# Performance work log

Hardware: AMD Instinct MI355X
Metric: run time of the kernel (lower is better)

## Reference

```python
import jax, jax.numpy as jnp
import numpy as np

N, E, G = 50000, 1600000, 512
IN, H = 16, 128


def setup_inputs() -> dict:
    key = jax.random.key(0)
    ks = jax.random.split(key, 10)
    x = jax.random.normal(ks[0], (N, IN), dtype=jnp.float32)
    edge_index = jax.random.randint(ks[1], (2, E), 0, N, dtype=jnp.int64)
    batch = jnp.sort(jax.random.randint(ks[2], (N,), 0, G, dtype=jnp.int64))
    s = lambda k, sh, fan: jax.random.normal(k, sh, dtype=jnp.float32) / np.sqrt(fan)
    return {
        "x": x, "edge_index": edge_index, "batch": batch,
        "W1": s(ks[3], (IN, H), IN), "b1": jnp.zeros((H,), jnp.float32),
        "W2": s(ks[4], (H, H), H), "b2": jnp.zeros((H,), jnp.float32),
        "Wlab": s(ks[5], (H, 1), H), "blab": jnp.zeros((1,), jnp.float32),
        "Wd1": s(ks[6], (H, 64), H), "bd1": jnp.zeros((64,), jnp.float32),
        "Wd2": s(ks[7], (64, 2), 64), "bd2": jnp.zeros((2,), jnp.float32),
    }


def _gcn_conv(x, src, dst, norm, W, b, num_nodes):
    # x' = sum_{(s,d) in E+selfloops} norm_e * (x W)[s] scattered to d, + b
    h = x @ W                                  # [N, H]
    msgs = h[src] * norm[:, None]              # [E+N, H]
    out = jax.ops.segment_sum(msgs, dst, num_segments=num_nodes)
    return out + b


def _forward(x, edge_index, batch, W1, b1, W2, b2, Wlab, blab, Wd1, bd1, Wd2, bd2):
    num_nodes = x.shape[0]
    loop = jnp.arange(num_nodes, dtype=edge_index.dtype)
    src = jnp.concatenate([edge_index[0], loop])
    dst = jnp.concatenate([edge_index[1], loop])
    # symmetric GCN normalization: deg computed at dst after self-loops
    deg = jax.ops.segment_sum(jnp.ones_like(dst, dtype=x.dtype), dst,
                              num_segments=num_nodes)
    dinv = jnp.where(deg > 0, jax.lax.rsqrt(deg), 0.0)
    norm = dinv[src] * dinv[dst]               # [E+N]

    h = jax.nn.relu(_gcn_conv(x, src, dst, norm, W1, b1, num_nodes))
    h = jax.nn.relu(_gcn_conv(h, src, dst, norm, W2, b2, num_nodes))

    # global mean pool over graphs
    sums = jax.ops.segment_sum(h, batch, num_segments=G)        # [G, H]
    cnts = jax.ops.segment_sum(jnp.ones((num_nodes,), h.dtype), batch,
                               num_segments=G)
    pooled = sums / jnp.maximum(cnts, 1.0)[:, None]

    label_out = jax.nn.sigmoid(pooled @ Wlab + blab)            # [G, 1]
    # grad_reverse is identity in the forward pass
    dom_out = jax.nn.relu(pooled @ Wd1 + bd1) @ Wd2 + bd2       # [G, 2]
    return label_out, dom_out


def reference(x, edge_index, batch, W1, b1, W2, b2, Wlab, blab, Wd1, bd1, Wd2, bd2):
    return _forward(x, edge_index, batch, W1, b1, W2, b2, Wlab, blab,
                    Wd1, bd1, Wd2, bd2)
```

## Files before the change

kernel.cpp:

```cpp
#include <hip/hip_runtime.h>
#include <math.h>


#define BCAP 12288

typedef __attribute__((ext_vector_type(8))) short short8;
typedef __attribute__((ext_vector_type(4))) float f32x4;

__device__ __forceinline__ void bf4acc(uint2 u, float* a) {
    a[0] += __uint_as_float(u.x << 16);
    a[1] += __uint_as_float(u.x & 0xffff0000u);
    a[2] += __uint_as_float(u.y << 16);
    a[3] += __uint_as_float(u.y & 0xffff0000u);
}

__device__ __forceinline__ unsigned short bf1(float a) {
    unsigned ua = __float_as_uint(a);
    return (unsigned short)((ua + 0x7fffu + ((ua >> 16) & 1u)) >> 16);
}

__global__ __launch_bounds__(256) void k_bfill(
        const int* __restrict__ ei, int* __restrict__ bcnt,
        unsigned* __restrict__ col1,
        const int* __restrict__ batch, int* __restrict__ gptr,
        float* __restrict__ gsum, const float* __restrict__ W2,
        unsigned short* __restrict__ W2bf,
        int E, int chunk, int NB, int N, int G) {
    __shared__ int bins[256];
    __shared__ int base[256];
    for (int t = threadIdx.x; t < NB; t += 256) bins[t] = 0;
    __syncthreads();
    const int e0 = blockIdx.x * chunk;
    int e1 = e0 + chunk; if (e1 > E) e1 = E;
    for (int j = e0 + (int)threadIdx.x; j < e1; j += 256)
        atomicAdd(&bins[ei[E + j] >> 8], 1);
    __syncthreads();
    for (int t = threadIdx.x; t < NB; t += 256) {
        base[t] = bins[t] ? atomicAdd(&bcnt[t], bins[t]) : 0;
        bins[t] = 0;
    }
    __syncthreads();
    for (int j = e0 + (int)threadIdx.x; j < e1; j += 256) {
        int d = ei[E + j];
        int s = ei[j];
        int b = d >> 8;
        int pos = base[b] + atomicAdd(&bins[b], 1);
        if (pos < BCAP)
            col1[(size_t)b * BCAP + pos] = ((unsigned)(d & 255) << 16) | (unsigned)s;
    }

    const int gid = blockIdx.x * 256 + threadIdx.x;
    const int gsz = gridDim.x * 256;
    for (int i = gid; i < G * 32; i += gsz)
        ((float4*)gsum)[i] = make_float4(0.f, 0.f, 0.f, 0.f);
    for (int i = gid; i < 16384; i += gsz) {
        const int f2 = i >> 7, f1 = i & 127;
        W2bf[i] = bf1(W2[f1 * 128 + f2]);
    }
    for (int g = gid; g <= G; g += gsz) {
        int lo = 0, hi = N;
        while (lo < hi) {
            int mid = (lo + hi) >> 1;
            if (batch[mid] < g) lo = mid + 1; else hi = mid;
        }
        gptr[g] = lo;
    }
}

__global__ __launch_bounds__(256) void k_bsort(const unsigned* __restrict__ col1,
                                               const int* __restrict__ bcnt,
                                               int* __restrict__ col,
                                               int* __restrict__ rowptr,
                                               float* __restrict__ dinv,
                                               const float* __restrict__ x,
                                               unsigned short* __restrict__ xsb,
                                               int N, int E, int NB) {
    __shared__ unsigned ec[BCAP];
    __shared__ int bins[256], sc[256];
    __shared__ float dvb[256];
    const int b = blockIdx.x, t = threadIdx.x;

    {
        int v = (t < NB) ? bcnt[t] : 0;
        bins[t] = v;
        __syncthreads();
        for (int off = 1; off < 256; off <<= 1) {
            int add = (t >= off) ? bins[t - off] : 0;
            __syncthreads();
            bins[t] += add;
            __syncthreads();
        }
    }
    const int s0 = (b == 0) ? 0 : bins[b - 1];
    int cnt = bcnt[b];
    if (cnt > BCAP) cnt = BCAP;
    __syncthreads();

    for (int i = t; i < cnt; i += 256) ec[i] = col1[(size_t)b * BCAP + i];
    bins[t] = 0;
    __syncthreads();
    for (int i = t; i < cnt; i += 256) atomicAdd(&bins[ec[i] >> 16], 1);
    __syncthreads();
    const int v = bins[t];
    sc[t] = v;
    __syncthreads();
    for (int off = 1; off < 256; off <<= 1) {
        int add = (t >= off) ? sc[t - off] : 0;
        __syncthreads();
        sc[t] += add;
        __syncthreads();
    }
    const int ex = sc[t] - v;
    __syncthreads();
    sc[t] = ex;
    bins[t] = 0;
    const float dv = rsqrtf((float)(v + 1));
    dvb[t] = dv;
    const int n0 = b * 256;
    if (n0 + t < N) {
        rowptr[n0 + t] = s0 + ex;
        dinv[n0 + t] = dv;
    }
    if (b == 0 && t == 0) rowptr[N] = E;
    __syncthreads();
    for (int i = t; i < cnt; i += 256) {
        unsigned e = ec[i];
        int dl = e >> 16;
        int p = sc[dl] + atomicAdd(&bins[dl], 1);
        col[s0 + p] = (int)(e & 0xffffu);
    }
    int nn = N - n0; if (nn > 256) nn = 256;
    const int lim = nn * 16;
    for (int i = t; i < lim; i += 256) {
        float vx = x[(size_t)n0 * 16 + i] * dvb[i >> 4];
        xsb[(size_t)n0 * 16 + i] = bf1(vx);
    }
}

__global__ __launch_bounds__(512, 4) void k_l12g(
        const int* __restrict__ rowptr, const int* __restrict__ col,
        const unsigned short* __restrict__ xsb,
        const float* __restrict__ dinv,
        const float* __restrict__ W1, const float* __restrict__ b1,
        const unsigned short* __restrict__ W2bf,
        unsigned short* __restrict__ ht1b, int N) {
    __shared__ __align__(16) unsigned short W2s[128 * 136];
    __shared__ __align__(16) unsigned short h1b[64 * 136];
    __shared__ __align__(16) float arow[64 * 16];
    __shared__ float dv[64];
    const int tid = threadIdx.x;
    const int n0 = blockIdx.x * 64;
    const int w = tid >> 6, lane = tid & 63;

    for (int i = tid; i < 2048; i += 512) {
        const int f2 = i >> 4, seg = i & 15;
        *(uint4*)&W2s[f2 * 136 + seg * 8] = ((const uint4*)W2bf)[i];
    }
    if (tid < 64) dv[tid] = (n0 + tid < N) ? dinv[n0 + tid] : 0.f;

    {
        const int nd = lane >> 3, sub = lane & 7;
        const int slot = sub >> 2, qq = sub & 3;
        const int j = w * 8 + nd;
        const int n = n0 + j;
        float a[4] = {0.f, 0.f, 0.f, 0.f};
        if (n < N) {
            const int r1 = rowptr[n + 1];
            for (int e = rowptr[n] + slot; e < r1; e += 2)
                bf4acc(*(const uint2*)(xsb + (size_t)col[e] * 16 + qq * 4), a);
        }
#pragma unroll
        for (int i = 0; i < 4; ++i) a[i] += __shfl_xor(a[i], 4);
        if (slot == 0) {
            if (n < N) {
                bf4acc(*(const uint2*)(xsb + (size_t)n * 16 + qq * 4), a);
                *(float4*)&arow[j * 16 + qq * 4] = make_float4(a[0], a[1], a[2], a[3]);
            } else {
                *(float4*)&arow[j * 16 + qq * 4] = make_float4(0.f, 0.f, 0.f, 0.f);
            }
        }
    }
    const int f = tid & 127, jg = tid >> 7;
    float w1r[16];
#pragma unroll
    for (int k = 0; k < 16; ++k) w1r[k] = W1[k * 128 + f];
    const float bias = b1[f];
    __syncthreads();

#pragma unroll 4
    for (int j = jg * 16; j < jg * 16 + 16; ++j) {
        float s = 0.f;
#pragma unroll
        for (int k = 0; k < 16; ++k) s += arow[j * 16 + k] * w1r[k];
        h1b[j * 136 + f] = bf1(fmaxf(dv[j] * s + bias, 0.f));
    }
    __syncthreads();

    const int mt = w & 3, nh = w >> 2;
    const int lm = lane & 15, quad = lane >> 4;
    f32x4 acc[4];
#pragma unroll
    for (int t = 0; t < 4; ++t) acc[t] = (f32x4){0.f, 0.f, 0.f, 0.f};
#pragma unroll
    for (int kb = 0; kb < 4; ++kb) {
        const short8 af = *(const short8*)&h1b[(mt * 16 + lm) * 136 + kb * 32 + quad * 8];
#pragma unroll
        for (int t = 0; t < 4; ++t) {
            const short8 bfv = *(const short8*)&W2s[(nh * 64 + t * 16 + lm) * 136 + kb * 32 + quad * 8];
            acc[t] = __builtin_amdgcn_mfma_f32_16x16x32_bf16(af, bfv, acc[t], 0, 0, 0);
        }
    }
#pragma unroll
    for (int t = 0; t < 4; ++t) {
        const int f2 = nh * 64 + t * 16 + lm;
#pragma unroll
        for (int r = 0; r < 4; ++r) {
            const int j = mt * 16 + quad * 4 + r;
            const int n = n0 + j;
            if (n < N)
                ht1b[(size_t)n * 128 + f2] = bf1(acc[t][r] * dv[j]);
        }
    }
}

__global__ __launch_bounds__(512) void k_gat128pool(
        const int* __restrict__ rowptr, const int* __restrict__ col,
        const unsigned short* __restrict__ ht1b,
        const float* __restrict__ dinv, const float* __restrict__ b2,
        const int* __restrict__ batch, float* __restrict__ gsum, int N) {
    __shared__ __align__(16) float h2s[8][128];
    __shared__ int bats[8];
    const int wave = threadIdx.x >> 6, lane = threadIdx.x & 63;
    const int half = lane >> 5, q = lane & 31;
    const int n = blockIdx.x * 8 + wave;
    float a[4] = {0.f, 0.f, 0.f, 0.f};
    if (n < N) {
        const int r0 = rowptr[n], r1 = rowptr[n + 1];
        int j = r0 + half;
        while (j + 6 < r1) {
            int s0 = col[j], s1 = col[j + 2], s2 = col[j + 4], s3 = col[j + 6];
            uint2 u0 = *(const uint2*)(ht1b + (size_t)s0 * 128 + q * 4);
            uint2 u1 = *(const uint2*)(ht1b + (size_t)s1 * 128 + q * 4);
            uint2 u2 = *(const uint2*)(ht1b + (size_t)s2 * 128 + q * 4);
            uint2 u3 = *(const uint2*)(ht1b + (size_t)s3 * 128 + q * 4);
            bf4acc(u0, a); bf4acc(u1, a); bf4acc(u2, a); bf4acc(u3, a);
            j += 8;
        }
        while (j < r1) {
            bf4acc(*(const uint2*)(ht1b + (size_t)col[j] * 128 + q * 4), a);
            j += 2;
        }
        if (half == 0)
            bf4acc(*(const uint2*)(ht1b + (size_t)n * 128 + q * 4), a);
    }
#pragma unroll
    for (int i = 0; i < 4; ++i) a[i] += __shfl_xor(a[i], 32);
    if (half == 0) {
        if (n < N) {
            const float d = dinv[n];
            const float4 bb = *(const float4*)(b2 + q * 4);
            h2s[wave][q * 4 + 0] = fmaxf(a[0] * d + bb.x, 0.f);
            h2s[wave][q * 4 + 1] = fmaxf(a[1] * d + bb.y, 0.f);
            h2s[wave][q * 4 + 2] = fmaxf(a[2] * d + bb.z, 0.f);
            h2s[wave][q * 4 + 3] = fmaxf(a[3] * d + bb.w, 0.f);
            if (q == 0) bats[wave] = batch[n];
        } else {
            h2s[wave][q * 4 + 0] = 0.f; h2s[wave][q * 4 + 1] = 0.f;
            h2s[wave][q * 4 + 2] = 0.f; h2s[wave][q * 4 + 3] = 0.f;
            if (q == 0) bats[wave] = -1;
        }
    }
    __syncthreads();
    if (threadIdx.x < 32) {
        const int qq = threadIdx.x;
        int bprev = bats[0];
        float4 acc4 = *(const float4*)&h2s[0][qq * 4];
#pragma unroll
        for (int wv = 1; wv < 8; ++wv) {
            const int bw = bats[wv];
            const float4 rv = *(const float4*)&h2s[wv][qq * 4];
            if (bw == bprev) {
                acc4.x += rv.x; acc4.y += rv.y; acc4.z += rv.z; acc4.w += rv.w;
            } else {
                if (bprev >= 0) {
                    float* gs = gsum + (size_t)bprev * 128 + qq * 4;
                    unsafeAtomicAdd(gs + 0, acc4.x); unsafeAtomicAdd(gs + 1, acc4.y);
                    unsafeAtomicAdd(gs + 2, acc4.z); unsafeAtomicAdd(gs + 3, acc4.w);
                }
                bprev = bw; acc4 = rv;
            }
        }
        if (bprev >= 0) {
            float* gs = gsum + (size_t)bprev * 128 + qq * 4;
            unsafeAtomicAdd(gs + 0, acc4.x); unsafeAtomicAdd(gs + 1, acc4.y);
            unsafeAtomicAdd(gs + 2, acc4.z); unsafeAtomicAdd(gs + 3, acc4.w);
        }
    }
}

__global__ __launch_bounds__(128) void k_head(
        const float* __restrict__ gsum, const int* __restrict__ gptr,
        const float* __restrict__ Wlab, const float* __restrict__ blab,
        const float* __restrict__ Wd1, const float* __restrict__ bd1,
        const float* __restrict__ Wd2, const float* __restrict__ bd2,
        float* __restrict__ out, int G) {
    __shared__ float sp[128];
    __shared__ float red[128];
    __shared__ float hd[64];
    const int g = blockIdx.x, t = threadIdx.x;
    const float cnt = (float)(gptr[g + 1] - gptr[g]);
    const float invc = 1.f / fmaxf(cnt, 1.f);
    const float pooled = gsum[g * 128 + t] * invc;
    sp[t] = pooled;
    red[t] = pooled * Wlab[t];
    __syncthreads();
    for (int off = 64; off > 0; off >>= 1) {
        if (t < off) red[t] += red[t + off];
        __syncthreads();
    }
    if (t == 0) {
        float z = red[0] + blab[0];
        out[g] = 1.f / (1.f + expf(-z));
    }
    if (t < 64) {
        float s = bd1[t];
        for (int f = 0; f < 128; ++f) s += sp[f] * Wd1[f * 64 + t];
        hd[t] = fmaxf(s, 0.f);
    }
    __syncthreads();
    if (t < 2) {
        float s = bd2[t];
        for (int j = 0; j < 64; ++j) s += hd[j] * Wd2[j * 2 + t];
        out[G + g * 2 + t] = s;
    }
}

extern "C" void kernel_launch(void* const* d_in, const int* in_sizes, int n_in,
                              void* d_out, int out_size, void* d_ws, size_t ws_size,
                              hipStream_t stream) {
    const float* x     = (const float*)d_in[0];
    const int*   ei    = (const int*)d_in[1];
    const int*   batch = (const int*)d_in[2];
    const float* W1    = (const float*)d_in[3];
    const float* b1    = (const float*)d_in[4];
    const float* W2    = (const float*)d_in[5];
    const float* b2    = (const float*)d_in[6];
    const float* Wlab  = (const float*)d_in[7];
    const float* blab  = (const float*)d_in[8];
    const float* Wd1   = (const float*)d_in[9];
    const float* bd1   = (const float*)d_in[10];
    const float* Wd2   = (const float*)d_in[11];
    const float* bd2   = (const float*)d_in[12];
    float* out = (float*)d_out;

    const int N = in_sizes[0] / 16;
    const int E = in_sizes[1] / 2;
    const int G = out_size / 3;
    const int NB = (N + 255) >> 8;

    char* p = (char*)d_ws;
    auto carve = [&](size_t bytes) {
        void* r = (void*)p;
        p += (bytes + 255) & ~(size_t)255;
        return r;
    };
    int*      bcnt   = (int*)     carve(256 * 4);
    unsigned* col1   = (unsigned*)carve((size_t)NB * BCAP * 4);
    int*      col    = (int*)     carve((size_t)E * 4);
    int*      rowptr = (int*)     carve((size_t)(N + 1) * 4);
    int*      gptr   = (int*)     carve((size_t)(G + 1) * 4);
    float*    dinv   = (float*)   carve((size_t)N * 4);
    unsigned short* xsb  = (unsigned short*)carve((size_t)N * 16 * 2);
    unsigned short* W2bf = (unsigned short*)carve(128 * 128 * 2);
    unsigned short* ht1b = (unsigned short*)carve((size_t)N * 128 * 2);
    float*    gsum   = (float*)   carve((size_t)G * 128 * 4);

    const int FB = 256;
    const int chunk = (E + FB - 1) / FB;

    hipMemsetAsync(bcnt, 0, 256 * 4, stream);
    k_bfill  <<<FB, 256, 0, stream>>>(ei, bcnt, col1, batch, gptr, gsum, W2,
                                      W2bf, E, chunk, NB, N, G);
    k_bsort  <<<NB, 256, 0, stream>>>(col1, bcnt, col, rowptr, dinv, x, xsb,
                                      N, E, NB);
    k_l12g   <<<(N + 63) / 64, 512, 0, stream>>>(rowptr, col, xsb, dinv,
                                                 W1, b1, W2bf, ht1b, N);
    k_gat128pool<<<(N + 7) / 8, 512, 0, stream>>>(rowptr, col, ht1b, dinv, b2,
                                                  batch, gsum, N);
    k_head   <<<G, 128, 0, stream>>>(gsum, gptr, Wlab, blab, Wd1, bd1, Wd2,
                                     bd2, out, G);
}
```

Measured before the change: 230.1 us.

## Split layer-2 gather-pool into two 64-column passes with 16-byte loads

The 128-feature neighbor gather-and-pool kernel is replaced by a kernel that handles one 64-column half of the features and is launched twice. Each wave now splits a node's edges over 8 lane groups and issues 16-byte loads per lane, so more edges are in flight and each pass touches a smaller slice of the bf16 feature table, which may fit the cache better. The cost is reading the CSR indices twice, two kernel launches, and more shuffle reductions.

```diff
diff --git a/kernel.cpp b/kernel.cpp
--- a/kernel.cpp
+++ b/kernel.cpp
@@ -12,6 +12,17 @@
     a[1] += __uint_as_float(u.x & 0xffff0000u);
     a[2] += __uint_as_float(u.y << 16);
     a[3] += __uint_as_float(u.y & 0xffff0000u);
+}
+
+__device__ __forceinline__ void bf8acc(uint4 u, float* a) {
+    a[0] += __uint_as_float(u.x << 16);
+    a[1] += __uint_as_float(u.x & 0xffff0000u);
+    a[2] += __uint_as_float(u.y << 16);
+    a[3] += __uint_as_float(u.y & 0xffff0000u);
+    a[4] += __uint_as_float(u.z << 16);
+    a[5] += __uint_as_float(u.z & 0xffff0000u);
+    a[6] += __uint_as_float(u.w << 16);
+    a[7] += __uint_as_float(u.w & 0xffff0000u);
 }
 
 __device__ __forceinline__ unsigned short bf1(float a) {
@@ -223,55 +234,69 @@
     }
 }
 
-__global__ __launch_bounds__(512) void k_gat128pool(
+__global__ __launch_bounds__(512) void k_gat64pool(
         const int* __restrict__ rowptr, const int* __restrict__ col,
         const unsigned short* __restrict__ ht1b,
         const float* __restrict__ dinv, const float* __restrict__ b2,
-        const int* __restrict__ batch, float* __restrict__ gsum, int N) {
-    __shared__ __align__(16) float h2s[8][128];
+        const int* __restrict__ batch, float* __restrict__ gsum,
+        int N, int c0) {
+    __shared__ __align__(16) float h2s[8][64];
     __shared__ int bats[8];
     const int wave = threadIdx.x >> 6, lane = threadIdx.x & 63;
-    const int half = lane >> 5, q = lane & 31;
+    const int oct = lane >> 3, t8 = lane & 7;
     const int n = blockIdx.x * 8 + wave;
-    float a[4] = {0.f, 0.f, 0.f, 0.f};
+    const unsigned short* hb = ht1b + c0 + t8 * 8;
+    float a[8] = {0.f, 0.f, 0.f, 0.f, 0.f, 0.f, 0.f, 0.f};
     if (n < N) {
-        const int r0 = rowptr[n], r1 = rowptr[n + 1];
-        int j = r0 + half;
-        while (j + 6 < r1) {
-            int s0 = col[j], s1 = col[j + 2], s2 = col[j + 4], s3 = col[j + 6];
-            uint2 u0 = *(const uint2*)(ht1b + (size_t)s0 * 128 + q * 4);
-            uint2 u1 = *(const uint2*)(ht1b + (size_t)s1 * 128 + q * 4);
-            uint2 u2 = *(const uint2*)(ht1b + (size_t)s2 * 128 + q * 4);
-            uint2 u3 = *(const uint2*)(ht1b + (size_t)s3 * 128 + q * 4);
-            bf4acc(u0, a); bf4acc(u1, a); bf4acc(u2, a); bf4acc(u3, a);
+        const int r1 = rowptr[n + 1];
+        int j = rowptr[n] + oct;
+        while (j + 24 < r1) {
+            const int s0 = col[j], s1 = col[j + 8];
+            const int s2 = col[j + 16], s3 = col[j + 24];
+            const uint4 u0 = *(const uint4*)(hb + (size_t)s0 * 128);
+            const uint4 u1 = *(const uint4*)(hb + (size_t)s1 * 128);
+            const uint4 u2 = *(const uint4*)(hb + (size_t)s2 * 128);
+            const uint4 u3 = *(const uint4*)(hb + (size_t)s3 * 128);
+            bf8acc(u0, a); bf8acc(u1, a); bf8acc(u2, a); bf8acc(u3, a);
+            j += 32;
+        }
+        while (j < r1) {
+            bf8acc(*(const uint4*)(hb + (size_t)col[j] * 128), a);
             j += 8;
         }
-        while (j < r1) {
-            bf4acc(*(const uint2*)(ht1b + (size_t)col[j] * 128 + q * 4), a);
-            j += 2;
-        }
-        if (half == 0)
-            bf4acc(*(const uint2*)(ht1b + (size_t)n * 128 + q * 4), a);
-    }
-#pragma unroll
-    for (int i = 0; i < 4; ++i) a[i] += __shfl_xor(a[i], 32);
-    if (half == 0) {
+        if (oct == 0)
+            bf8acc(*(const uint4*)(hb + (size_t)n * 128), a);
+    }
+#pragma unroll
+    for (int i = 0; i < 8; ++i) {
+        a[i] += __shfl_xor(a[i], 8);
+        a[i] += __shfl_xor(a[i], 16);
+        a[i] += __shfl_xor(a[i], 32);
+    }
+    if (oct == 0) {
         if (n < N) {
             const float d = dinv[n];
-            const float4 bb = *(const float4*)(b2 + q * 4);
-            h2s[wave][q * 4 + 0] = fmaxf(a[0] * d + bb.x, 0.f);
-            h2s[wave][q * 4 + 1] = fmaxf(a[1] * d + bb.y, 0.f);
-            h2s[wave][q * 4 + 2] = fmaxf(a[2] * d + bb.z, 0.f);
-            h2s[wave][q * 4 + 3] = fmaxf(a[3] * d + bb.w, 0.f);
-            if (q == 0) bats[wave] = batch[n];
+            const float4 bb0 = *(const float4*)(b2 + c0 + t8 * 8);
+            const float4 bb1 = *(const float4*)(b2 + c0 + t8 * 8 + 4);
+            const float4 v0 = make_float4(fmaxf(a[0] * d + bb0.x, 0.f),
+                                          fmaxf(a[1] * d + bb0.y, 0.f),
+                                          fmaxf(a[2] * d + bb0.z, 0.f),
+                                          fmaxf(a[3] * d + bb0.w, 0.f));
+            const float4 v1 = make_float4(fmaxf(a[4] * d + bb1.x, 0.f),
+                                          fmaxf(a[5] * d + bb1.y, 0.f),
+                                          fmaxf(a[6] * d + bb1.z, 0.f),
+                                          fmaxf(a[7] * d + bb1.w, 0.f));
+            *(float4*)&h2s[wave][t8 * 8] = v0;
+            *(float4*)&h2s[wave][t8 * 8 + 4] = v1;
+            if (t8 == 0) bats[wave] = batch[n];
         } else {
-            h2s[wave][q * 4 + 0] = 0.f; h2s[wave][q * 4 + 1] = 0.f;
-            h2s[wave][q * 4 + 2] = 0.f; h2s[wave][q * 4 + 3] = 0.f;
-            if (q == 0) bats[wave] = -1;
-        }
-    }
-    __syncthreads();
-    if (threadIdx.x < 32) {
+            *(float4*)&h2s[wave][t8 * 8] = make_float4(0.f, 0.f, 0.f, 0.f);
+            *(float4*)&h2s[wave][t8 * 8 + 4] = make_float4(0.f, 0.f, 0.f, 0.f);
+            if (t8 == 0) bats[wave] = -1;
+        }
+    }
+    __syncthreads();
+    if (threadIdx.x < 16) {
         const int qq = threadIdx.x;
         int bprev = bats[0];
         float4 acc4 = *(const float4*)&h2s[0][qq * 4];
@@ -283,7 +308,7 @@
                 acc4.x += rv.x; acc4.y += rv.y; acc4.z += rv.z; acc4.w += rv.w;
             } else {
                 if (bprev >= 0) {
-                    float* gs = gsum + (size_t)bprev * 128 + qq * 4;
+                    float* gs = gsum + (size_t)bprev * 128 + c0 + qq * 4;
                     unsafeAtomicAdd(gs + 0, acc4.x); unsafeAtomicAdd(gs + 1, acc4.y);
                     unsafeAtomicAdd(gs + 2, acc4.z); unsafeAtomicAdd(gs + 3, acc4.w);
                 }
@@ -291,7 +316,7 @@
             }
         }
         if (bprev >= 0) {
-            float* gs = gsum + (size_t)bprev * 128 + qq * 4;
+            float* gs = gsum + (size_t)bprev * 128 + c0 + qq * 4;
             unsafeAtomicAdd(gs + 0, acc4.x); unsafeAtomicAdd(gs + 1, acc4.y);
             unsafeAtomicAdd(gs + 2, acc4.z); unsafeAtomicAdd(gs + 3, acc4.w);
         }
@@ -385,8 +410,10 @@
                                       N, E, NB);
     k_l12g   <<<(N + 63) / 64, 512, 0, stream>>>(rowptr, col, xsb, dinv,
                                                  W1, b1, W2bf, ht1b, N);
-    k_gat128pool<<<(N + 7) / 8, 512, 0, stream>>>(rowptr, col, ht1b, dinv, b2,
-                                                  batch, gsum, N);
+    k_gat64pool<<<(N + 7) / 8, 512, 0, stream>>>(rowptr, col, ht1b, dinv, b2,
+                                                 batch, gsum, N, 0);
+    k_gat64pool<<<(N + 7) / 8, 512, 0, stream>>>(rowptr, col, ht1b, dinv, b2,
+                                                 batch, gsum, N, 64);
     k_head   <<<G, 128, 0, stream>>>(gsum, gptr, Wlab, blab, Wd1, bd1, Wd2,
                                      bd2, out, G);
 }
```

After: 248.3 us. 1.08x slower.

## Locally sort edge tiles in LDS before bucket scatter for coalesced writes

Applied to the files above, without the earlier changes.

The bucket-fill kernel now loads fixed 4096-edge tiles into shared memory and counting-sorts them by destination bucket with a block-wide prefix scan. It then writes each bucket's run contiguously into the global bucket arrays, replacing the scattered per-edge global writes. The grid grows from 256 blocks to about 391, and edges are read from global memory once instead of twice. The cost is extra shared-memory passes, a serial scan with many barriers, and higher LDS use per block, which may lower occupancy.

```diff
diff --git a/kernel.cpp b/kernel.cpp
--- a/kernel.cpp
+++ b/kernel.cpp
@@ -3,6 +3,7 @@
 
 
 #define BCAP 12288
+#define TILE 4096
 
 typedef __attribute__((ext_vector_type(8))) short short8;
 typedef __attribute__((ext_vector_type(4))) float f32x4;
@@ -25,31 +26,55 @@
         const int* __restrict__ batch, int* __restrict__ gptr,
         float* __restrict__ gsum, const float* __restrict__ W2,
         unsigned short* __restrict__ W2bf,
-        int E, int chunk, int NB, int N, int G) {
-    __shared__ int bins[256];
-    __shared__ int base[256];
-    for (int t = threadIdx.x; t < NB; t += 256) bins[t] = 0;
-    __syncthreads();
-    const int e0 = blockIdx.x * chunk;
-    int e1 = e0 + chunk; if (e1 > E) e1 = E;
-    for (int j = e0 + (int)threadIdx.x; j < e1; j += 256)
-        atomicAdd(&bins[ei[E + j] >> 8], 1);
-    __syncthreads();
-    for (int t = threadIdx.x; t < NB; t += 256) {
-        base[t] = bins[t] ? atomicAdd(&bcnt[t], bins[t]) : 0;
-        bins[t] = 0;
-    }
-    __syncthreads();
-    for (int j = e0 + (int)threadIdx.x; j < e1; j += 256) {
-        int d = ei[E + j];
-        int s = ei[j];
-        int b = d >> 8;
-        int pos = base[b] + atomicAdd(&bins[b], 1);
+        int E, int NB, int N, int G) {
+    __shared__ unsigned ev[TILE];
+    __shared__ unsigned es[TILE];
+    __shared__ int bins[256], scn[256], cur[256], gbase[256];
+    const int t = threadIdx.x;
+    const int e0 = blockIdx.x * TILE;
+    int cnt = E - e0; if (cnt > TILE) cnt = TILE;
+
+    bins[t] = 0;
+    __syncthreads();
+    for (int i = t; i < cnt; i += 256) {
+        const int d = ei[E + e0 + i];
+        const int s = ei[e0 + i];
+        const unsigned b = (unsigned)d >> 8;
+        ev[i] = (b << 24) | ((unsigned)(d & 255) << 16) | (unsigned)s;
+        atomicAdd(&bins[b], 1);
+    }
+    __syncthreads();
+    const int v = bins[t];
+    scn[t] = v;
+    __syncthreads();
+    for (int off = 1; off < 256; off <<= 1) {
+        int add = (t >= off) ? scn[t - off] : 0;
+        __syncthreads();
+        scn[t] += add;
+        __syncthreads();
+    }
+    const int ex = scn[t] - v;
+    __syncthreads();
+    scn[t] = ex;
+    cur[t] = 0;
+    gbase[t] = v ? atomicAdd(&bcnt[t], v) : 0;
+    __syncthreads();
+    for (int i = t; i < cnt; i += 256) {
+        const unsigned e = ev[i];
+        const int b = e >> 24;
+        const int p = scn[b] + atomicAdd(&cur[b], 1);
+        es[p] = e;
+    }
+    __syncthreads();
+    for (int i = t; i < cnt; i += 256) {
+        const unsigned e = es[i];
+        const int b = e >> 24;
+        const int pos = gbase[b] + (i - scn[b]);
         if (pos < BCAP)
-            col1[(size_t)b * BCAP + pos] = ((unsigned)(d & 255) << 16) | (unsigned)s;
-    }
-
-    const int gid = blockIdx.x * 256 + threadIdx.x;
+            col1[(size_t)b * BCAP + pos] = e & 0xffffffu;
+    }
+
+    const int gid = blockIdx.x * 256 + t;
     const int gsz = gridDim.x * 256;
     for (int i = gid; i < G * 32; i += gsz)
         ((float4*)gsum)[i] = make_float4(0.f, 0.f, 0.f, 0.f);
@@ -375,12 +400,11 @@
     unsigned short* ht1b = (unsigned short*)carve((size_t)N * 128 * 2);
     float*    gsum   = (float*)   carve((size_t)G * 128 * 4);
 
-    const int FB = 256;
-    const int chunk = (E + FB - 1) / FB;
+    const int FB = (E + TILE - 1) / TILE;
 
     hipMemsetAsync(bcnt, 0, 256 * 4, stream);
     k_bfill  <<<FB, 256, 0, stream>>>(ei, bcnt, col1, batch, gptr, gsum, W2,
-                                      W2bf, E, chunk, NB, N, G);
+                                      W2bf, E, NB, N, G);
     k_bsort  <<<NB, 256, 0, stream>>>(col1, bcnt, col, rowptr, dinv, x, xsb,
                                       N, E, NB);
     k_l12g   <<<(N + 63) / 64, 512, 0, stream>>>(rowptr, col, xsb, dinv,
```

New measurement: 222.9 us. 3.1% less time.
